# Kernel tuning notes

Measured on AMD Instinct MI355X. Metric: run time of the kernel, lower is better.

The kernel has to match this reference:

```python
import jax, jax.numpy as jnp
import numpy as np

K = 7      # involution kernel size
G = 16     # groups
EPS = 1e-5 # BatchNorm eps (torch default)


def setup_inputs() -> dict:
    key = jax.random.key(0)
    ks = jax.random.split(key, 5)
    N, C, H, W = 4, 256, 56, 56
    Cr = C // 4            # ratio=4 reduction channels
    KKG = K * K * G        # 784 dynamic-kernel channels
    x = jax.random.normal(ks[0], (N, C, H, W), dtype=jnp.float32)
    w1 = jax.random.normal(ks[1], (Cr, C), dtype=jnp.float32) * 0.05
    b1 = jax.random.normal(ks[2], (Cr,), dtype=jnp.float32) * 0.05
    gamma = jnp.ones((Cr,), dtype=jnp.float32)
    beta = jnp.zeros((Cr,), dtype=jnp.float32)
    mean = jnp.zeros((Cr,), dtype=jnp.float32)
    var = jnp.ones((Cr,), dtype=jnp.float32)
    w2 = jax.random.normal(ks[3], (KKG, Cr), dtype=jnp.float32) * 0.05
    b2 = jax.random.normal(ks[4], (KKG,), dtype=jnp.float32) * 0.05
    return {"x": x, "w1": w1, "b1": b1, "gamma": gamma, "beta": beta,
            "mean": mean, "var": var, "w2": w2, "b2": b2}


def _involution(x, w1, b1, gamma, beta, mean, var, w2, b2):
    N, C, H, W = x.shape
    pad = K // 2
    # --- kernel-generating branch (stride=1 => AvgPool is identity) ---
    t = jnp.einsum('nchw,oc->nohw', x, w1) + b1[None, :, None, None]   # 1x1 conv
    inv_std = jax.lax.rsqrt(var + EPS)
    t = (t - mean[None, :, None, None]) * (inv_std * gamma)[None, :, None, None] \
        + beta[None, :, None, None]                                    # BatchNorm (inference)
    t = jax.nn.relu(t)
    ker = jnp.einsum('nohw,ko->nkhw', t, w2) + b2[None, :, None, None] # (N, K*K*G, H, W)
    ker = ker.reshape(N, G, K * K, H, W)                               # per-group dyn kernels
    # --- unfold (im2col), torch layout: (N, C, K*K, H, W), kk = kh*K + kw ---
    xp = jnp.pad(x, ((0, 0), (0, 0), (pad, pad), (pad, pad)))
    patches = jnp.stack(
        [xp[:, :, i:i + H, j:j + W] for i in range(K) for j in range(K)], axis=2)
    patches = patches.reshape(N, G, C // G, K * K, H, W)
    # --- per-pixel weighted sum over kernel positions ---
    out = jnp.einsum('ngckhw,ngkhw->ngchw', patches, ker)
    return out.reshape(N, C, H, W)


def reference(x, w1, b1, gamma, beta, mean, var, w2, b2):
    return _involution(x, w1, b1, gamma, beta, mean, var, w2, b2)
```

## Files before the change

### kernel.cpp

```cpp
#include <hip/hip_runtime.h>


namespace {
constexpr int Nn  = 4;
constexpr int Cc  = 256;
constexpr int Hh  = 56;
constexpr int Ww  = 56;
constexpr int HW  = Hh * Ww;
constexpr int NPX = Nn * HW;
constexpr int KK  = 49;
}

extern "C" __global__ void __launch_bounds__(256, 8)
k1_conv_bn_relu(const float* __restrict__ x,  const float* __restrict__ w1,
                const float* __restrict__ b1, const float* __restrict__ gamma,
                const float* __restrict__ beta, const float* __restrict__ mean,
                const float* __restrict__ var,  float* __restrict__ t)
{
    const int lane = threadIdx.x & 63;
    const int wv   = __builtin_amdgcn_readfirstlane(threadIdx.x >> 6);
    const int px   = blockIdx.x * 64 + lane;
    const int o0   = __builtin_amdgcn_readfirstlane(((int)blockIdx.y * 4 + wv) * 4);

    const int n  = px / HW;
    const int hw = px - n * HW;
    const float* xb = x + (size_t)n * Cc * HW + hw;

    float a0 = 0.f, a1 = 0.f, a2 = 0.f, a3 = 0.f;

#pragma unroll 8
    for (int c = 0; c < Cc; ++c) {
        const float xv = xb[(size_t)c * HW];
        a0 = fmaf(xv, w1[(o0 + 0) * Cc + c], a0);
        a1 = fmaf(xv, w1[(o0 + 1) * Cc + c], a1);
        a2 = fmaf(xv, w1[(o0 + 2) * Cc + c], a2);
        a3 = fmaf(xv, w1[(o0 + 3) * Cc + c], a3);
    }

    float accs[4] = {a0, a1, a2, a3};
#pragma unroll
    for (int oo = 0; oo < 4; ++oo) {
        const int o = o0 + oo;
        const float inv = rsqrtf(var[o] + 1e-5f);
        const float sc  = gamma[o] * inv;
        const float sh  = fmaf(b1[o] - mean[o], sc, beta[o]);
        float v = fmaf(accs[oo], sc, sh);
        t[(size_t)o * NPX + px] = v > 0.f ? v : 0.f;
    }
}

extern "C" __global__ void __launch_bounds__(256, 4)
k2_involution(const float* __restrict__ x,  const float* __restrict__ t,
              const float* __restrict__ w2, const float* __restrict__ b2,
              float* __restrict__ out)
{
    __shared__ float red[4][16][64];

    const int lane = threadIdx.x & 63;
    const int wv   = __builtin_amdgcn_readfirstlane(threadIdx.x >> 6);
    const int nh   = blockIdx.x;
    const int n    = nh / Hh;
    const int h    = nh - n * Hh;
    const int g    = __builtin_amdgcn_readfirstlane((int)blockIdx.y);
    const int wcl  = lane < Ww ? lane : (Ww - 1);
    const int pxb  = nh * Ww;

    float treg[64];
#pragma unroll
    for (int o = 0; o < 64; ++o)
        treg[o] = t[o * NPX + pxb + wcl];
#pragma unroll
    for (int o = 0; o < 64; ++o)
        asm volatile("" : "+v"(treg[o]));

    float acc[16];
#pragma unroll
    for (int i = 0; i < 16; ++i) acc[i] = 0.f;

    const float* xg  = x  + (size_t)n * Cc * HW + (size_t)(g * 16) * HW;
    const float* w2g = w2 + g * KK * 64;
    const float* b2g = b2 + g * KK;

    for (int k = wv; k < KK; k += 4) {
        const int kh = k / 7;
        const int kw = k - kh * 7;
        const int hh = h + kh - 3;
        if (hh < 0 || hh >= Hh) continue;
        const float* xrow  = xg + hh * Ww;
        const float* w2row = w2g + k * 64;
        float p0 = 0.f, p1 = 0.f, p2 = 0.f, p3 = 0.f;
#pragma unroll
        for (int o = 0; o < 64; o += 4) {
            p0 = fmaf(treg[o + 0], w2row[o + 0], p0);
            p1 = fmaf(treg[o + 1], w2row[o + 1], p1);
            p2 = fmaf(treg[o + 2], w2row[o + 2], p2);
            p3 = fmaf(treg[o + 3], w2row[o + 3], p3);
        }
        const float kerk = ((p0 + p1) + (p2 + p3)) + b2g[k];
        const int ww = lane + kw - 3;
        if (ww >= 0 && ww < Ww) {
#pragma unroll
            for (int c = 0; c < 16; ++c)
                acc[c] = fmaf(xrow[(size_t)c * HW + ww], kerk, acc[c]);
        }
    }

#pragma unroll
    for (int c = 0; c < 16; ++c)
        red[wv][c][lane] = acc[c];
    __syncthreads();

    if (lane < Ww) {
        float* og = out + (size_t)n * Cc * HW + (size_t)(g * 16) * HW + h * Ww + lane;
#pragma unroll
        for (int j = 0; j < 4; ++j) {
            const int c = wv * 4 + j;
            const float s = red[0][c][lane] + red[1][c][lane]
                          + red[2][c][lane] + red[3][c][lane];
            og[c * HW] = s;
        }
    }
}

extern "C" void kernel_launch(void* const* d_in, const int* in_sizes, int n_in,
                              void* d_out, int out_size, void* d_ws, size_t ws_size,
                              hipStream_t stream)
{
    const float* x     = (const float*)d_in[0];
    const float* w1    = (const float*)d_in[1];
    const float* b1    = (const float*)d_in[2];
    const float* gamma = (const float*)d_in[3];
    const float* beta  = (const float*)d_in[4];
    const float* mean  = (const float*)d_in[5];
    const float* var   = (const float*)d_in[6];
    const float* w2    = (const float*)d_in[7];
    const float* b2    = (const float*)d_in[8];

    float* t   = (float*)d_ws;
    float* out = (float*)d_out;

    k1_conv_bn_relu<<<dim3(NPX / 64, 4), 256, 0, stream>>>(
        x, w1, b1, gamma, beta, mean, var, t);
    k2_involution<<<dim3(Nn * Hh, 16), 256, 0, stream>>>(
        x, t, w2, b2, out);
}
```

Before: 83.37 us.

## Split k1 channel reduction across waves; restructure k2 kernel generation loop order

k1 now gives each wave a quarter of the input channels for 8 output channels and reduces the partial sums through shared memory. That cuts the serial reduction length per thread, and the grid in y doubles. k2 no longer holds all 64 t values in registers. It streams t in chunks of 4 and accumulates all 13 dynamic-kernel values per wave up front, which lowers register pressure and separates kernel generation from the gather-FMA loop. The cost is extra LDS traffic and a barrier in k1, and repeated loads of w2 inside the inner loop in k2.

```diff
diff --git a/kernel.cpp b/kernel.cpp
--- a/kernel.cpp
+++ b/kernel.cpp
@@ -9,6 +9,7 @@
 constexpr int HW  = Hh * Ww;
 constexpr int NPX = Nn * HW;
 constexpr int KK  = 49;
+constexpr int Cr  = 64;
 }
 
 extern "C" __global__ void __launch_bounds__(256, 8)
@@ -17,34 +18,45 @@
                 const float* __restrict__ beta, const float* __restrict__ mean,
                 const float* __restrict__ var,  float* __restrict__ t)
 {
+    __shared__ float red[4][8][64];
+
     const int lane = threadIdx.x & 63;
     const int wv   = __builtin_amdgcn_readfirstlane(threadIdx.x >> 6);
     const int px   = blockIdx.x * 64 + lane;
-    const int o0   = __builtin_amdgcn_readfirstlane(((int)blockIdx.y * 4 + wv) * 4);
+    const int o0   = __builtin_amdgcn_readfirstlane((int)blockIdx.y * 8);
 
     const int n  = px / HW;
     const int hw = px - n * HW;
     const float* xb = x + (size_t)n * Cc * HW + hw;
+    const int c0 = wv * 64;
 
-    float a0 = 0.f, a1 = 0.f, a2 = 0.f, a3 = 0.f;
+    float acc[8];
+#pragma unroll
+    for (int i = 0; i < 8; ++i) acc[i] = 0.f;
 
 #pragma unroll 8
-    for (int c = 0; c < Cc; ++c) {
+    for (int cc = 0; cc < 64; ++cc) {
+        const int c = c0 + cc;
         const float xv = xb[(size_t)c * HW];
-        a0 = fmaf(xv, w1[(o0 + 0) * Cc + c], a0);
-        a1 = fmaf(xv, w1[(o0 + 1) * Cc + c], a1);
-        a2 = fmaf(xv, w1[(o0 + 2) * Cc + c], a2);
-        a3 = fmaf(xv, w1[(o0 + 3) * Cc + c], a3);
+#pragma unroll
+        for (int oo = 0; oo < 8; ++oo)
+            acc[oo] = fmaf(xv, w1[(o0 + oo) * Cc + c], acc[oo]);
     }
 
-    float accs[4] = {a0, a1, a2, a3};
 #pragma unroll
-    for (int oo = 0; oo < 4; ++oo) {
-        const int o = o0 + oo;
+    for (int oo = 0; oo < 8; ++oo) red[wv][oo][lane] = acc[oo];
+    __syncthreads();
+
+#pragma unroll
+    for (int j = 0; j < 2; ++j) {
+        const int oo = wv * 2 + j;
+        const int o  = o0 + oo;
+        const float s = red[0][oo][lane] + red[1][oo][lane]
+                      + red[2][oo][lane] + red[3][oo][lane];
         const float inv = rsqrtf(var[o] + 1e-5f);
         const float sc  = gamma[o] * inv;
         const float sh  = fmaf(b1[o] - mean[o], sc, beta[o]);
-        float v = fmaf(accs[oo], sc, sh);
+        const float v   = fmaf(s, sc, sh);
         t[(size_t)o * NPX + px] = v > 0.f ? v : 0.f;
     }
 }
@@ -65,43 +77,57 @@
     const int wcl  = lane < Ww ? lane : (Ww - 1);
     const int pxb  = nh * Ww;
 
-    float treg[64];
+    const float* tp  = t  + pxb + wcl;
+    const float* w2g = w2 + g * KK * Cr;
+    const float* b2g = b2 + g * KK;
+
+    float ker[13];
 #pragma unroll
-    for (int o = 0; o < 64; ++o)
-        treg[o] = t[o * NPX + pxb + wcl];
+    for (int j = 0; j < 13; ++j) {
+        int k = wv + 4 * j; if (k > KK - 1) k = KK - 1;
+        ker[j] = b2g[k];
+    }
+
+#pragma unroll 2
+    for (int o = 0; o < Cr; o += 4) {
+        const float tv0 = tp[(size_t)(o + 0) * NPX];
+        const float tv1 = tp[(size_t)(o + 1) * NPX];
+        const float tv2 = tp[(size_t)(o + 2) * NPX];
+        const float tv3 = tp[(size_t)(o + 3) * NPX];
 #pragma unroll
-    for (int o = 0; o < 64; ++o)
-        asm volatile("" : "+v"(treg[o]));
+        for (int j = 0; j < 13; ++j) {
+            int k = wv + 4 * j; if (k > KK - 1) k = KK - 1;
+            const float* wr = w2g + k * Cr + o;
+            float kj = ker[j];
+            kj = fmaf(tv0, wr[0], kj);
+            kj = fmaf(tv1, wr[1], kj);
+            kj = fmaf(tv2, wr[2], kj);
+            kj = fmaf(tv3, wr[3], kj);
+            ker[j] = kj;
+        }
+    }
 
     float acc[16];
 #pragma unroll
     for (int i = 0; i < 16; ++i) acc[i] = 0.f;
 
-    const float* xg  = x  + (size_t)n * Cc * HW + (size_t)(g * 16) * HW;
-    const float* w2g = w2 + g * KK * 64;
-    const float* b2g = b2 + g * KK;
+    const float* xg = x + (size_t)n * Cc * HW + (size_t)(g * 16) * HW;
 
-    for (int k = wv; k < KK; k += 4) {
+#pragma unroll
+    for (int j = 0; j < 13; ++j) {
+        const int k = wv + 4 * j;
+        if (k >= KK) break;
         const int kh = k / 7;
         const int kw = k - kh * 7;
         const int hh = h + kh - 3;
         if (hh < 0 || hh >= Hh) continue;
-        const float* xrow  = xg + hh * Ww;
-        const float* w2row = w2g + k * 64;
-        float p0 = 0.f, p1 = 0.f, p2 = 0.f, p3 = 0.f;
-#pragma unroll
-        for (int o = 0; o < 64; o += 4) {
-            p0 = fmaf(treg[o + 0], w2row[o + 0], p0);
-            p1 = fmaf(treg[o + 1], w2row[o + 1], p1);
-            p2 = fmaf(treg[o + 2], w2row[o + 2], p2);
-            p3 = fmaf(treg[o + 3], w2row[o + 3], p3);
-        }
-        const float kerk = ((p0 + p1) + (p2 + p3)) + b2g[k];
         const int ww = lane + kw - 3;
+        const float kerv = ker[j];
+        const float* xr = xg + hh * Ww + ww;
         if (ww >= 0 && ww < Ww) {
 #pragma unroll
             for (int c = 0; c < 16; ++c)
-                acc[c] = fmaf(xrow[(size_t)c * HW + ww], kerk, acc[c]);
+                acc[c] = fmaf(xr[(size_t)c * HW], kerv, acc[c]);
         }
     }
 
@@ -139,7 +165,7 @@
     float* t   = (float*)d_ws;
     float* out = (float*)d_out;
 
-    k1_conv_bn_relu<<<dim3(NPX / 64, 4), 256, 0, stream>>>(
+    k1_conv_bn_relu<<<dim3(NPX / 64, 8), 256, 0, stream>>>(
         x, w1, b1, gamma, beta, mean, var, t);
     k2_involution<<<dim3(Nn * Hh, 16), 256, 0, stream>>>(
         x, t, w2, b2, out);
```

New measurement: 96.98 us. 1.16x slower.
